# Kernel tuning notes

Measured on AMD Instinct MI355X. Metric: run time of the kernel, lower is better.

The kernel has to match this reference:

```python
import math
import jax, jax.numpy as jnp
import numpy as np

ALPH = 0.8

def setup_inputs() -> dict:
    key = jax.random.key(0)
    k1, k2 = jax.random.split(key)
    B, C, N, T = 64, 64, 500, 48
    x = jax.random.normal(k1, (B, C, N, T), dtype=jnp.float32)
    s = jax.random.uniform(k2, (N, N), dtype=jnp.float32)
    return {"x": x, "s": s}

def reference(x, s):
    # x: [B, C, N, T], s: [N, N]
    B, C, N, T = x.shape
    # Row sums of the (never materialized) [N*T, N*T] supra-laplacian:
    # block row i, node v -> s.sum(axis=1)[v] + (T-1-i)*alph
    s_rowsum = s.sum(axis=1)                              # [N]
    time_term = (T - 1 - jnp.arange(T, dtype=jnp.float32)) * ALPH  # [T]
    rowsum = (time_term[:, None] + s_rowsum[None, :]).reshape(-1)  # [T*N], k = i*N+v
    # Faithful to original: x flattened as [B, C, N*T] (k = n*T + t), multiplied
    # elementwise by rowsum[k] (the 'bcn,nm->bcn' einsum reduces to this).
    x_window = x.reshape(B, C, N * T)
    x_window = jax.nn.relu(x_window * rowsum / math.sqrt(C))
    adj_dyn = jax.nn.softmax(x_window, axis=-1)            # [B, C, N*T]
    x_w_s = adj_dyn.reshape(B, C, N, T).sum(-1)            # [B, C, N]
    gram = jnp.einsum('bcn,bcm->bnm', x_w_s, x_w_s)        # [B, N, N]
    A_l = jax.nn.softmax(jax.nn.relu(gram) / math.sqrt(C), axis=-1)
    return A_l
```

## Files before the change

### kernel.cpp

```cpp
#include <hip/hip_runtime.h>
#include <math.h>

#define NN 500
#define TT 48
#define NT 24000
#define NF4 6000

typedef float f4v __attribute__((ext_vector_type(4)));

__global__ void k_srow(const float* __restrict__ s, float* __restrict__ srow) {
    int r = blockIdx.x;
    int l = threadIdx.x;
    float v = 0.f;
    for (int j = l; j < NN; j += 64) v += s[r * NN + j];
    #pragma unroll
    for (int o = 32; o; o >>= 1) v += __shfl_xor(v, o);
    if (l == 0) srow[r] = v;
}

__global__ void k_rs(const float* __restrict__ srow, float* __restrict__ rs) {
    int k = blockIdx.x * 256 + threadIdx.x;
    if (k < NT) {
        int i = k / NN;
        int v = k - i * NN;
        rs[k] = (float)(TT - 1 - i) * 0.8f + srow[v];
    }
}

__launch_bounds__(512, 8)
__global__ void k_p1(const float* __restrict__ x, const float* __restrict__ rs,
                     float* __restrict__ xws) {
    __shared__ float p[6144];
    __shared__ float redm[8], reds[8];
    int bc = blockIdx.x;
    int tid = threadIdx.x;
    int w = tid >> 6, l = tid & 63;
    int f0 = w * 768 + l;

    const f4v* xp = (const f4v*)x + (size_t)bc * NF4;
    const f4v* rp = (const f4v*)rs;

    float sf[12], ml[12];
    float m = 0.f;

    #pragma unroll
    for (int i = 0; i < 9; i++) {
        int f = f0 + i * 64;
        f4v xv = __builtin_nontemporal_load(xp + f);
        f4v rv = rp[f];
        float y0 = fmaxf(xv.x * rv.x * 0.125f, 0.f);
        float y1 = fmaxf(xv.y * rv.y * 0.125f, 0.f);
        float y2 = fmaxf(xv.z * rv.z * 0.125f, 0.f);
        float y3 = fmaxf(xv.w * rv.w * 0.125f, 0.f);
        float mm = fmaxf(fmaxf(y0, y1), fmaxf(y2, y3));
        sf[i] = __expf(y0 - mm) + __expf(y1 - mm)
              + __expf(y2 - mm) + __expf(y3 - mm);
        ml[i] = mm;
        m = fmaxf(m, mm);
    }
    #pragma unroll
    for (int i = 9; i < 12; i++) {
        int f = f0 + i * 64;
        int fc = (f < NF4) ? f : (NF4 - 1);
        float msk = (f < NF4) ? 1.f : 0.f;
        f4v xv = __builtin_nontemporal_load(xp + fc);
        f4v rv = rp[fc];
        float y0 = fmaxf(xv.x * rv.x * 0.125f, 0.f);
        float y1 = fmaxf(xv.y * rv.y * 0.125f, 0.f);
        float y2 = fmaxf(xv.z * rv.z * 0.125f, 0.f);
        float y3 = fmaxf(xv.w * rv.w * 0.125f, 0.f);
        float mm = fmaxf(fmaxf(y0, y1), fmaxf(y2, y3));
        float sfi = __expf(y0 - mm) + __expf(y1 - mm)
                  + __expf(y2 - mm) + __expf(y3 - mm);
        sf[i] = sfi * msk;
        ml[i] = mm;
        m = fmaxf(m, mm);
    }

    #pragma unroll
    for (int o = 32; o; o >>= 1) m = fmaxf(m, __shfl_xor(m, o));
    if (l == 0) redm[w] = m;
    __syncthreads();
    float M = redm[0];
    #pragma unroll
    for (int i = 1; i < 8; i++) M = fmaxf(M, redm[i]);

    float tot = 0.f;
    #pragma unroll
    for (int i = 0; i < 12; i++) {
        float cf = sf[i] * __expf(ml[i] - M);
        p[f0 + i * 64] = cf;
        tot += cf;
    }
    #pragma unroll
    for (int o = 32; o; o >>= 1) tot += __shfl_xor(tot, o);
    if (l == 0) reds[w] = tot;
    __syncthreads();
    float Z = 0.f;
    #pragma unroll
    for (int i = 0; i < 8; i++) Z += reds[i];

    if (tid < NN) {
        const float* pp = p + tid * 12;
        float sn = 0.f;
        #pragma unroll
        for (int j = 0; j < 12; j++) sn += pp[j];
        xws[(size_t)bc * NN + tid] = sn / Z;
    }
}

__launch_bounds__(512, 4)
__global__ void k_p2(const float* __restrict__ xws, float* __restrict__ out) {
    __shared__ __align__(16) float Xs[32 * NN + 16];
    int b = blockIdx.y;
    int rt8 = blockIdx.x;
    int tid = threadIdx.x;

    int rt = tid >> 6, cx = tid & 63;
    int r0 = rt8 * 64 + rt * 8;
    int cb0 = cx * 4, cb1 = cx * 4 + 256;

    float acc[8][8];
    #pragma unroll
    for (int i = 0; i < 8; i++)
        #pragma unroll
        for (int j = 0; j < 8; j++) acc[i][j] = 0.f;

    for (int cbk = 0; cbk < 2; cbk++) {
        const float4* src4 = (const float4*)(xws + ((size_t)b * 64 + 32 * cbk) * NN);
        __syncthreads();
        #pragma unroll
        for (int i = 0; i < 8; i++) {
            int idx = tid + i * 512;
            if (idx < 4000) ((float4*)Xs)[idx] = src4[idx];
        }
        if (tid < 16) Xs[32 * NN + tid] = 0.f;
        __syncthreads();

        #pragma unroll 4
        for (int c = 0; c < 32; c++) {
            const float* row = Xs + c * NN;
            float4 a0 = *(const float4*)(row + r0);
            float4 a1 = *(const float4*)(row + r0 + 4);
            float4 b0 = *(const float4*)(row + cb0);
            float4 b1 = *(const float4*)(row + cb1);
            float av[8] = {a0.x, a0.y, a0.z, a0.w, a1.x, a1.y, a1.z, a1.w};
            float bv[8] = {b0.x, b0.y, b0.z, b0.w, b1.x, b1.y, b1.z, b1.w};
            #pragma unroll
            for (int i = 0; i < 8; i++)
                #pragma unroll
                for (int j = 0; j < 8; j++)
                    acc[i][j] = fmaf(av[i], bv[j], acc[i][j]);
        }
    }

    bool c1v = (cx <= 60);
    size_t ob = (size_t)b * (NN * NN);
    #pragma unroll 1
    for (int ri = 0; ri < 8; ri++) {
        int r = r0 + ri;
        if (r >= NN) break;
        float u[8];
        #pragma unroll
        for (int j = 0; j < 8; j++) u[j] = fmaxf(acc[ri][j], 0.f) * 0.125f;
        float mx = fmaxf(fmaxf(u[0], u[1]), fmaxf(u[2], u[3]));
        if (c1v) mx = fmaxf(mx, fmaxf(fmaxf(u[4], u[5]), fmaxf(u[6], u[7])));
        #pragma unroll
        for (int o = 32; o; o >>= 1) mx = fmaxf(mx, __shfl_xor(mx, o));

        float e[8];
        float es = 0.f;
        #pragma unroll
        for (int j = 0; j < 4; j++) { e[j] = __expf(u[j] - mx); es += e[j]; }
        if (c1v) {
            #pragma unroll
            for (int j = 4; j < 8; j++) { e[j] = __expf(u[j] - mx); es += e[j]; }
        }
        #pragma unroll
        for (int o = 32; o; o >>= 1) es += __shfl_xor(es, o);
        float inv = 1.f / es;

        float4 w0 = make_float4(e[0] * inv, e[1] * inv, e[2] * inv, e[3] * inv);
        *(float4*)(out + ob + (size_t)r * NN + cb0) = w0;
        if (c1v) {
            float4 w1 = make_float4(e[4] * inv, e[5] * inv, e[6] * inv, e[7] * inv);
            *(float4*)(out + ob + (size_t)r * NN + cb1) = w1;
        }
    }
}

extern "C" void kernel_launch(void* const* d_in, const int* in_sizes, int n_in,
                              void* d_out, int out_size, void* d_ws, size_t ws_size,
                              hipStream_t stream) {
    const float* x = (const float*)d_in[0];
    const float* s = (const float*)d_in[1];
    float* out = (float*)d_out;
    float* wsf = (float*)d_ws;

    float* srow = wsf;
    float* rs   = wsf + 1024;
    float* xws  = wsf + 32768;

    k_srow<<<NN, 64, 0, stream>>>(s, srow);
    k_rs<<<(NT + 255) / 256, 256, 0, stream>>>(srow, rs);
    k_p1<<<64 * 64, 512, 0, stream>>>(x, rs, xws);
    dim3 g2(8, 64);
    k_p2<<<g2, 512, 0, stream>>>(xws, out);
}
```

Baseline: 177.4 us.

## Fuse rowsum computation into softmax kernel using shared-memory srow

```diff
diff --git a/kernel.cpp b/kernel.cpp
--- a/kernel.cpp
+++ b/kernel.cpp
@@ -5,8 +5,6 @@
 #define TT 48
 #define NT 24000
 #define NF4 6000
-
-typedef float f4v __attribute__((ext_vector_type(4)));
 
 __global__ void k_srow(const float* __restrict__ s, float* __restrict__ srow) {
     int r = blockIdx.x;
@@ -18,27 +16,21 @@
     if (l == 0) srow[r] = v;
 }
 
-__global__ void k_rs(const float* __restrict__ srow, float* __restrict__ rs) {
-    int k = blockIdx.x * 256 + threadIdx.x;
-    if (k < NT) {
-        int i = k / NN;
-        int v = k - i * NN;
-        rs[k] = (float)(TT - 1 - i) * 0.8f + srow[v];
-    }
-}
-
-__launch_bounds__(512, 8)
-__global__ void k_p1(const float* __restrict__ x, const float* __restrict__ rs,
+__launch_bounds__(512, 4)
+__global__ void k_p1(const float* __restrict__ x, const float* __restrict__ srow,
                      float* __restrict__ xws) {
     __shared__ float p[6144];
+    __shared__ __align__(16) float sr[512];
     __shared__ float redm[8], reds[8];
     int bc = blockIdx.x;
     int tid = threadIdx.x;
     int w = tid >> 6, l = tid & 63;
     int f0 = w * 768 + l;
 
-    const f4v* xp = (const f4v*)x + (size_t)bc * NF4;
-    const f4v* rp = (const f4v*)rs;
+    if (tid < NN) sr[tid] = srow[tid];
+    __syncthreads();
+
+    const float4* xp = (const float4*)x + (size_t)bc * NF4;
 
     float sf[12], ml[12];
     float m = 0.f;
@@ -46,12 +38,16 @@
     #pragma unroll
     for (int i = 0; i < 9; i++) {
         int f = f0 + i * 64;
-        f4v xv = __builtin_nontemporal_load(xp + f);
-        f4v rv = rp[f];
-        float y0 = fmaxf(xv.x * rv.x * 0.125f, 0.f);
-        float y1 = fmaxf(xv.y * rv.y * 0.125f, 0.f);
-        float y2 = fmaxf(xv.z * rv.z * 0.125f, 0.f);
-        float y3 = fmaxf(xv.w * rv.w * 0.125f, 0.f);
+        int kk = 4 * f;
+        int ti = kk / 500;
+        int v  = kk - ti * 500;
+        float tt = (float)(TT - 1 - ti) * 0.8f;
+        float4 sv = *(const float4*)(sr + v);
+        float4 xv = xp[f];
+        float y0 = fmaxf(xv.x * (tt + sv.x) * 0.125f, 0.f);
+        float y1 = fmaxf(xv.y * (tt + sv.y) * 0.125f, 0.f);
+        float y2 = fmaxf(xv.z * (tt + sv.z) * 0.125f, 0.f);
+        float y3 = fmaxf(xv.w * (tt + sv.w) * 0.125f, 0.f);
         float mm = fmaxf(fmaxf(y0, y1), fmaxf(y2, y3));
         sf[i] = __expf(y0 - mm) + __expf(y1 - mm)
               + __expf(y2 - mm) + __expf(y3 - mm);
@@ -63,12 +59,16 @@
         int f = f0 + i * 64;
         int fc = (f < NF4) ? f : (NF4 - 1);
         float msk = (f < NF4) ? 1.f : 0.f;
-        f4v xv = __builtin_nontemporal_load(xp + fc);
-        f4v rv = rp[fc];
-        float y0 = fmaxf(xv.x * rv.x * 0.125f, 0.f);
-        float y1 = fmaxf(xv.y * rv.y * 0.125f, 0.f);
-        float y2 = fmaxf(xv.z * rv.z * 0.125f, 0.f);
-        float y3 = fmaxf(xv.w * rv.w * 0.125f, 0.f);
+        int kk = 4 * fc;
+        int ti = kk / 500;
+        int v  = kk - ti * 500;
+        float tt = (float)(TT - 1 - ti) * 0.8f;
+        float4 sv = *(const float4*)(sr + v);
+        float4 xv = xp[fc];
+        float y0 = fmaxf(xv.x * (tt + sv.x) * 0.125f, 0.f);
+        float y1 = fmaxf(xv.y * (tt + sv.y) * 0.125f, 0.f);
+        float y2 = fmaxf(xv.z * (tt + sv.z) * 0.125f, 0.f);
+        float y3 = fmaxf(xv.w * (tt + sv.w) * 0.125f, 0.f);
         float mm = fmaxf(fmaxf(y0, y1), fmaxf(y2, y3));
         float sfi = __expf(y0 - mm) + __expf(y1 - mm)
                   + __expf(y2 - mm) + __expf(y3 - mm);
@@ -198,12 +198,10 @@
     float* wsf = (float*)d_ws;
 
     float* srow = wsf;
-    float* rs   = wsf + 1024;
     float* xws  = wsf + 32768;
 
     k_srow<<<NN, 64, 0, stream>>>(s, srow);
-    k_rs<<<(NT + 255) / 256, 256, 0, stream>>>(srow, rs);
-    k_p1<<<64 * 64, 512, 0, stream>>>(x, rs, xws);
+    k_p1<<<64 * 64, 512, 0, stream>>>(x, srow, xws);
     dim3 g2(8, 64);
     k_p2<<<g2, 512, 0, stream>>>(xws, out);
 }
```

Result: faster. 166.8 us (-6.0%).
